# Optimization experiments

Hardware: AMD Instinct MI355X
Metric: run time of the kernel (lower is better)

## Reference

```python
import jax, jax.numpy as jnp
import numpy as np

DIM = 128
WS = 8            # window_size
NH = 4            # num_heads
SHIFT = 4         # shift_size
HD = DIM // NH    # head_dim = 32
SCALE = HD ** (-0.5)
N = WS * WS       # tokens per window = 64


def _rel_pos_index():
    # Static relative-position index, [N, N], values in [0, (2*WS-1)^2)
    coords = np.stack(np.meshgrid(np.arange(WS), np.arange(WS), indexing='ij'))  # [2,WS,WS]
    cf = coords.reshape(2, -1)                                                   # [2,N]
    rel = (cf[:, :, None] - cf[:, None, :]).transpose(1, 2, 0)                   # [N,N,2]
    rel[:, :, 0] += WS - 1
    rel[:, :, 1] += WS - 1
    rel[:, :, 0] *= 2 * WS - 1
    return rel.sum(-1)


def _shift_mask(H, W):
    # Static shifted-window attention mask, [nW, N, N] with 0 / -100 entries
    img = np.zeros((H, W))
    cnt = 0
    for hs in (slice(0, -WS), slice(-WS, -SHIFT), slice(-SHIFT, None)):
        for ws in (slice(0, -WS), slice(-WS, -SHIFT), slice(-SHIFT, None)):
            img[hs, ws] = cnt
            cnt += 1
    mw = img.reshape(H // WS, WS, W // WS, WS).transpose(0, 2, 1, 3).reshape(-1, N)
    am = mw[:, None, :] - mw[:, :, None]
    return np.where(am != 0, -100.0, 0.0).astype(np.float32)


def setup_inputs() -> dict:
    key = jax.random.key(0)
    ks = jax.random.split(key, 5)
    B, H, W = 8, 256, 256
    x = jax.random.normal(ks[0], (B, DIM, H, W), dtype=jnp.float32)
    qkv_w = jax.random.normal(ks[1], (3 * DIM, DIM), dtype=jnp.float32) * (DIM ** -0.5)
    proj_w = jax.random.normal(ks[2], (DIM, DIM), dtype=jnp.float32) * (DIM ** -0.5)
    proj_b = jax.random.normal(ks[3], (DIM,), dtype=jnp.float32) * 0.01
    bias_table = jax.random.normal(ks[4], ((2 * WS - 1) ** 2, NH), dtype=jnp.float32) * 0.02
    return {"x": x, "qkv_w": qkv_w, "proj_w": proj_w, "proj_b": proj_b,
            "bias_table": bias_table}


def reference(x, qkv_w, proj_w, proj_b, bias_table):
    B, C, H, W = x.shape
    # cyclic shift
    x = jnp.roll(x, (-SHIFT, -SHIFT), axis=(2, 3))
    # 1x1 conv qkv == channel matmul
    qkv = jnp.einsum('bchw,oc->bohw', x, qkv_w)  # [B, 3C, H, W]
    nWh, nWw = H // WS, W // WS
    nW = nWh * nWw
    qkv = qkv.reshape(B, 3, NH, HD, nWh, WS, nWw, WS)
    qkv = qkv.transpose(1, 0, 4, 6, 2, 5, 7, 3)          # [3,B,nWh,nWw,NH,WS,WS,HD]
    qkv = qkv.reshape(3, B * nW, NH, N, HD)
    q, k, v = qkv[0], qkv[1], qkv[2]
    attn = jnp.einsum('wnqd,wnkd->wnqk', q, k) * SCALE   # [B*nW, NH, N, N]
    # relative position bias gather
    rpi = _rel_pos_index().reshape(-1)
    bias = bias_table[rpi].reshape(N, N, NH).transpose(2, 0, 1)  # [NH,N,N]
    attn = attn + bias[None]
    # shifted-window mask
    mask = jnp.asarray(_shift_mask(H, W))                # [nW, N, N]
    attn = attn.reshape(B, nW, NH, N, N) + mask[None, :, None]
    attn = jax.nn.softmax(attn, axis=-1).reshape(B * nW, NH, N, N)
    out = jnp.einsum('wnqk,wnkd->wnqd', attn, v)         # [B*nW, NH, N, HD]
    out = out.reshape(B, nWh, nWw, NH, WS, WS, HD)
    out = out.transpose(0, 3, 6, 1, 4, 2, 5).reshape(B, C, H, W)
    out = jnp.einsum('bchw,oc->bohw', out, proj_w) + proj_b[None, :, None, None]
    out = jnp.roll(out, (SHIFT, SHIFT), axis=(2, 3))
    return out
```

## Files before the change

### kernel.cpp

```cpp
#include <hip/hip_runtime.h>

typedef __attribute__((ext_vector_type(8))) short short8;
typedef __attribute__((ext_vector_type(4))) unsigned short ushort4v;
typedef __attribute__((ext_vector_type(4))) float f32x4;

#define SCALE_F 0.17677669529663687f

__device__ __forceinline__ unsigned short f2bf(float f){
  unsigned u = __builtin_bit_cast(unsigned, f);
  u += 0x7fffu + ((u >> 16) & 1u);
  return (unsigned short)(u >> 16);
}
__device__ __forceinline__ float bf2f(unsigned short h){
  unsigned u = ((unsigned)h) << 16;
  return __builtin_bit_cast(float, u);
}


template<bool WSB>
__global__ void __launch_bounds__(256, 2)
swin_fused(const float* __restrict__ x, const float* __restrict__ qkvw_f,
           const float* __restrict__ projw_f, const float* __restrict__ projb,
           const float* __restrict__ btab, const unsigned short* __restrict__ wbf,
           float* __restrict__ out)
{
  __shared__ __align__(16) unsigned char sm[65536];
  const int tid  = threadIdx.x;
  const int lane = tid & 63, wv = tid >> 6;
  const int lr = lane & 15, lg = lane >> 4;

  const int bid = blockIdx.x;
  const int sw  = ((bid & 7) << 10) | (bid >> 3);
  const int b   = sw >> 10;
  const int wh  = (sw >> 5) & 31, ww = sw & 31;
  const int hb  = wh * 8 + 4, wb = ww * 8 + 4;
  const bool h31 = (wh == 31), w31 = (ww == 31);

  {
    const int t  = tid & 63;
    const int gh = (hb + (t >> 3)) & 255;
    const int gw = (wb + (t & 7)) & 255;
    const float* px = x + (((b * 128) << 16) + (gh << 8) + gw);
    const int c0b = (tid >> 6) * 8;
    #pragma unroll
    for (int it = 0; it < 4; ++it) {
      const int c0 = c0b + it * 32;
      const float* p = px + (c0 << 16);
      short8 v;
      #pragma unroll
      for (int cc = 0; cc < 8; ++cc) v[cc] = (short)f2bf(p[cc << 16]);
      *(short8*)(sm + t * 256 + ((2 * c0) ^ ((t & 7) << 4))) = v;
    }
  }
  __syncthreads();

  {
    short8 Bf[16];
    #pragma unroll
    for (int nt = 0; nt < 4; ++nt)
      #pragma unroll
      for (int kk = 0; kk < 4; ++kk) {
        const int t = nt * 16 + lr;
        Bf[nt * 4 + kk] = *(short8*)(sm + t * 256 + ((64 * kk + 16 * lg) ^ ((t & 7) << 4)));
      }
    #pragma unroll
    for (int jj = 0; jj < 6; ++jj) {
      const int mt = wv + 4 * jj;
      const int orow = mt * 16 + lr;
      short8 Af[4];
      #pragma unroll
      for (int kk = 0; kk < 4; ++kk) {
        const int off = orow * 128 + kk * 32 + 8 * lg;
        if constexpr (WSB) {
          Af[kk] = *(const short8*)(wbf + off);
        } else {
          const float* p = qkvw_f + off;
          short8 r;
          #pragma unroll
          for (int e = 0; e < 8; ++e) r[e] = (short)f2bf(p[e]);
          Af[kk] = r;
        }
      }
      f32x4 acc[4];
      #pragma unroll
      for (int nt = 0; nt < 4; ++nt) {
        acc[nt] = (f32x4)(0.f);
        #pragma unroll
        for (int kk = 0; kk < 4; ++kk)
          acc[nt] = __builtin_amdgcn_mfma_f32_16x16x32_bf16(Af[kk], Bf[nt * 4 + kk], acc[nt], 0, 0, 0);
      }
      if (mt < 16) {
        const int base = (mt < 8) ? 16384 : 32768;
        const int c0 = ((mt & 7) * 16) + 4 * lg;
        #pragma unroll
        for (int nt = 0; nt < 4; ++nt) {
          const int t = nt * 16 + lr;
          ushort4v pk;
          #pragma unroll
          for (int r = 0; r < 4; ++r) pk[r] = f2bf(acc[nt][r]);
          *(ushort4v*)(sm + base + t * 256 + ((2 * c0) ^ ((t & 7) << 4))) = pk;
        }
      } else {
        const int c0 = (mt - 16) * 16 + 4 * lg;
        #pragma unroll
        for (int nt = 0; nt < 4; ++nt) {
          const int t = nt * 16 + lr;
          #pragma unroll
          for (int r = 0; r < 4; ++r) {
            const int c = c0 + r;
            *(unsigned short*)(sm + 49152 + c * 128 + ((2 * t) ^ ((c & 7) << 4))) = f2bf(acc[nt][r]);
          }
        }
      }
    }
  }
  __syncthreads();

  f32x4 accpv[8];
  #pragma unroll
  for (int z = 0; z < 8; ++z) accpv[z] = (f32x4)(0.f);

  #pragma unroll
  for (int h = 0; h < 4; ++h) {
    {
      const int cb = 64 * h + 16 * lg;
      const int ktc = wv * 16 + lr;
      const short8 kb = *(short8*)(sm + 32768 + ktc * 256 + (cb ^ ((ktc & 7) << 4)));
      const int ki = ktc >> 3, kj = ktc & 7;
      #pragma unroll
      for (int mt = 0; mt < 4; ++mt) {
        const int q = mt * 16 + lr;
        const short8 qa = *(short8*)(sm + 16384 + q * 256 + (cb ^ ((q & 7) << 4)));
        f32x4 sacc = __builtin_amdgcn_mfma_f32_16x16x32_bf16(qa, kb, (f32x4)(0.f), 0, 0, 0);
        #pragma unroll
        for (int r = 0; r < 4; ++r) {
          const int qrow = mt * 16 + 4 * lg + r;
          const int qi = qrow >> 3, qj = qrow & 7;
          float s = sacc[r] * SCALE_F;
          s += btab[((qi - ki + 7) * 15 + (qj - kj + 7)) * 4 + h];
          const bool bad = (h31 && ((qi >= 4) != (ki >= 4))) || (w31 && ((qj >= 4) != (kj >= 4)));
          s += bad ? -100.f : 0.f;
          *(unsigned short*)(sm + qrow * 128 + ((2 * ktc) ^ ((qrow & 7) << 4))) = f2bf(s);
        }
      }
    }
    __syncthreads();
    {
      const int srow = tid >> 2, sq = tid & 3;
      const int swz = (srow & 7) << 4;
      const short8 s0 = *(short8*)(sm + srow * 128 + ((sq * 32) ^ swz));
      const short8 s1 = *(short8*)(sm + srow * 128 + ((sq * 32 + 16) ^ swz));
      float v[16];
      #pragma unroll
      for (int e = 0; e < 8; ++e) { v[e] = bf2f((unsigned short)s0[e]); v[e + 8] = bf2f((unsigned short)s1[e]); }
      float mx = v[0];
      #pragma unroll
      for (int e = 1; e < 16; ++e) mx = fmaxf(mx, v[e]);
      mx = fmaxf(mx, __shfl_xor(mx, 1));
      mx = fmaxf(mx, __shfl_xor(mx, 2));
      float sum = 0.f;
      #pragma unroll
      for (int e = 0; e < 16; ++e) { v[e] = __expf(v[e] - mx); sum += v[e]; }
      sum += __shfl_xor(sum, 1);
      sum += __shfl_xor(sum, 2);
      const float inv = 1.f / sum;
      short8 p0, p1;
      #pragma unroll
      for (int e = 0; e < 8; ++e) { p0[e] = (short)f2bf(v[e] * inv); p1[e] = (short)f2bf(v[e + 8] * inv); }
      *(short8*)(sm + 8192 + srow * 128 + ((sq * 32) ^ swz)) = p0;
      *(short8*)(sm + 8192 + srow * 128 + ((sq * 32 + 16) ^ swz)) = p1;
    }
    __syncthreads();
    {
      const int q = wv * 16 + lr;
      const int qs_ = (q & 7) << 4;
      const short8 pa0 = *(short8*)(sm + 8192 + q * 128 + ((16 * lg) ^ qs_));
      const short8 pa1 = *(short8*)(sm + 8192 + q * 128 + ((64 + 16 * lg) ^ qs_));
      #pragma unroll
      for (int nd = 0; nd < 2; ++nd) {
        const int c = h * 32 + nd * 16 + lr;
        const int cs = (c & 7) << 4;
        const short8 vb0 = *(short8*)(sm + 49152 + c * 128 + ((16 * lg) ^ cs));
        const short8 vb1 = *(short8*)(sm + 49152 + c * 128 + ((64 + 16 * lg) ^ cs));
        f32x4 a = accpv[h * 2 + nd];
        a = __builtin_amdgcn_mfma_f32_16x16x32_bf16(pa0, vb0, a, 0, 0, 0);
        a = __builtin_amdgcn_mfma_f32_16x16x32_bf16(pa1, vb1, a, 0, 0, 0);
        accpv[h * 2 + nd] = a;
      }
    }
  }

  {
    #pragma unroll
    for (int h = 0; h < 4; ++h)
      #pragma unroll
      for (int nd = 0; nd < 2; ++nd) {
        const int c = h * 32 + nd * 16 + lr;
        const f32x4 a = accpv[h * 2 + nd];
        #pragma unroll
        for (int r = 0; r < 4; ++r) {
          const int t = wv * 16 + 4 * lg + r;
          *(unsigned short*)(sm + 16384 + t * 256 + ((2 * c) ^ ((t & 7) << 4))) = f2bf(a[r]);
        }
      }
  }
  __syncthreads();

  {
    short8 Aa[16];
    #pragma unroll
    for (int mt = 0; mt < 4; ++mt)
      #pragma unroll
      for (int kk = 0; kk < 4; ++kk) {
        const int t = mt * 16 + lr;
        Aa[mt * 4 + kk] = *(short8*)(sm + 16384 + t * 256 + ((64 * kk + 16 * lg) ^ ((t & 7) << 4)));
      }
    #pragma unroll
    for (int ntl = 0; ntl < 2; ++ntl) {
      const int nt = wv + 4 * ntl;
      const int o = nt * 16 + lr;
      short8 Bw[4];
      #pragma unroll
      for (int kk = 0; kk < 4; ++kk) {
        const int coff = kk * 32 + 8 * lg;
        if constexpr (WSB) {
          Bw[kk] = *(const short8*)(wbf + 49152 + o * 128 + coff);
        } else {
          const float* p = projw_f + o * 128 + coff;
          short8 r;
          #pragma unroll
          for (int e = 0; e < 8; ++e) r[e] = (short)f2bf(p[e]);
          Bw[kk] = r;
        }
      }
      const float pb = projb[o];
      #pragma unroll
      for (int mt = 0; mt < 4; ++mt) {
        f32x4 acc = (f32x4)(0.f);
        #pragma unroll
        for (int kk = 0; kk < 4; ++kk)
          acc = __builtin_amdgcn_mfma_f32_16x16x32_bf16(Aa[mt * 4 + kk], Bw[kk], acc, 0, 0, 0);
        const int t0 = mt * 16 + 4 * lg;
        const int gh = (hb + (t0 >> 3)) & 255;
        const int gw0 = (wb + (t0 & 7)) & 255;
        f32x4 ov;
        ov[0] = acc[0] + pb; ov[1] = acc[1] + pb; ov[2] = acc[2] + pb; ov[3] = acc[3] + pb;
        *(f32x4*)(out + (((b * 128 + o) << 16) + (gh << 8) + gw0)) = ov;
      }
    }
  }
}

__global__ void prep_weights(const float* __restrict__ qw, const float* __restrict__ pw,
                             unsigned short* __restrict__ wsb)
{
  const int i = blockIdx.x * 256 + threadIdx.x;
  const int idx = i * 4;
  const float* src = (idx < 49152) ? (qw + idx) : (pw + (idx - 49152));
  f32x4 v = *(const f32x4*)src;
  ushort4v o;
  #pragma unroll
  for (int e = 0; e < 4; ++e) o[e] = f2bf(v[e]);
  *(ushort4v*)(wsb + idx) = o;
}

extern "C" void kernel_launch(void* const* d_in, const int* in_sizes, int n_in,
                              void* d_out, int out_size, void* d_ws, size_t ws_size,
                              hipStream_t stream) {
  const float* x     = (const float*)d_in[0];
  const float* qkvw  = (const float*)d_in[1];
  const float* projw = (const float*)d_in[2];
  const float* projb = (const float*)d_in[3];
  const float* btab  = (const float*)d_in[4];
  float* out = (float*)d_out;

  if (ws_size >= 131072) {
    unsigned short* wsb = (unsigned short*)d_ws;
    prep_weights<<<64, 256, 0, stream>>>(qkvw, projw, wsb);
    swin_fused<true><<<8192, 256, 0, stream>>>(x, qkvw, projw, projb, btab, wsb, out);
  } else {
    swin_fused<false><<<8192, 256, 0, stream>>>(x, qkvw, projw, projb, btab, nullptr, out);
  }
}
```

Measured before the change: 394.3 us.

## Compute QKV per head inside attention loop to shrink LDS and raise occupancy

```diff
diff --git a/kernel.cpp b/kernel.cpp
--- a/kernel.cpp
+++ b/kernel.cpp
@@ -3,8 +3,10 @@
 typedef __attribute__((ext_vector_type(8))) short short8;
 typedef __attribute__((ext_vector_type(4))) unsigned short ushort4v;
 typedef __attribute__((ext_vector_type(4))) float f32x4;
+typedef __attribute__((ext_vector_type(4))) unsigned int uint4v;
 
 #define SCALE_F 0.17677669529663687f
+#define SW(t) ((((t) ^ ((t) >> 3)) & 7) << 4)
 
 __device__ __forceinline__ unsigned short f2bf(float f){
   unsigned u = __builtin_bit_cast(unsigned, f);
@@ -15,16 +17,30 @@
   unsigned u = ((unsigned)h) << 16;
   return __builtin_bit_cast(float, u);
 }
+__device__ __forceinline__ unsigned cvtpk(float a, float b){
+  unsigned w;
+  asm("v_cvt_pk_bf16_f32 %0, %1, %2" : "=v"(w) : "v"(a), "v"(b));
+  return w;
+}
+__device__ __forceinline__ void st_pk4(void* p, f32x4 a){
+  uint2 u; u.x = cvtpk(a[0], a[1]); u.y = cvtpk(a[2], a[3]);
+  *(uint2*)p = u;
+}
 
 
 template<bool WSB>
-__global__ void __launch_bounds__(256, 2)
+__global__ void __launch_bounds__(256, 4)
 swin_fused(const float* __restrict__ x, const float* __restrict__ qkvw_f,
            const float* __restrict__ projw_f, const float* __restrict__ projb,
            const float* __restrict__ btab, const unsigned short* __restrict__ wbf,
            float* __restrict__ out)
 {
-  __shared__ __align__(16) unsigned char sm[65536];
+  __shared__ __align__(16) unsigned char sm[39424];
+  unsigned char* const smq = sm + 16384;
+  unsigned char* const smk = sm + 21504;
+  unsigned char* const smv = sm + 26624;
+  unsigned char* const smS = sm + 31232;
+
   const int tid  = threadIdx.x;
   const int lane = tid & 63, wv = tid >> 6;
   const int lr = lane & 15, lg = lane >> 4;
@@ -37,119 +53,122 @@
   const bool h31 = (wh == 31), w31 = (ww == 31);
 
   {
-    const int t  = tid & 63;
-    const int gh = (hb + (t >> 3)) & 255;
-    const int gw = (wb + (t & 7)) & 255;
-    const float* px = x + (((b * 128) << 16) + (gh << 8) + gw);
-    const int c0b = (tid >> 6) * 8;
-    #pragma unroll
-    for (int it = 0; it < 4; ++it) {
-      const int c0 = c0b + it * 32;
-      const float* p = px + (c0 << 16);
-      short8 v;
-      #pragma unroll
-      for (int cc = 0; cc < 8; ++cc) v[cc] = (short)f2bf(p[cc << 16]);
-      *(short8*)(sm + t * 256 + ((2 * c0) ^ ((t & 7) << 4))) = v;
+    #pragma unroll
+    for (int it = 0; it < 8; ++it) {
+      const int f = tid + 256 * it;
+      const int c    = f >> 4;
+      const int rr   = (f >> 1) & 7;
+      const int half = f & 1;
+      const int gh = (hb + rr) & 255;
+      const int gw = (wb + 4 * half) & 255;
+      const f32x4 v = *(const f32x4*)(x + (((b * 128 + c) << 16) + (gh << 8) + gw));
+      const int t0 = rr * 8 + 4 * half;
+      #pragma unroll
+      for (int e = 0; e < 4; ++e) {
+        const int t = t0 + e;
+        *(unsigned short*)(sm + t * 256 + ((2 * c) ^ SW(t))) = f2bf(v[e]);
+      }
     }
   }
   __syncthreads();
 
-  {
-    short8 Bf[16];
-    #pragma unroll
-    for (int nt = 0; nt < 4; ++nt)
-      #pragma unroll
-      for (int kk = 0; kk < 4; ++kk) {
-        const int t = nt * 16 + lr;
-        Bf[nt * 4 + kk] = *(short8*)(sm + t * 256 + ((64 * kk + 16 * lg) ^ ((t & 7) << 4)));
-      }
-    #pragma unroll
-    for (int jj = 0; jj < 6; ++jj) {
-      const int mt = wv + 4 * jj;
-      const int orow = mt * 16 + lr;
-      short8 Af[4];
-      #pragma unroll
-      for (int kk = 0; kk < 4; ++kk) {
-        const int off = orow * 128 + kk * 32 + 8 * lg;
-        if constexpr (WSB) {
-          Af[kk] = *(const short8*)(wbf + off);
-        } else {
-          const float* p = qkvw_f + off;
-          short8 r;
-          #pragma unroll
-          for (int e = 0; e < 8; ++e) r[e] = (short)f2bf(p[e]);
-          Af[kk] = r;
-        }
-      }
-      f32x4 acc[4];
-      #pragma unroll
-      for (int nt = 0; nt < 4; ++nt) {
-        acc[nt] = (f32x4)(0.f);
-        #pragma unroll
-        for (int kk = 0; kk < 4; ++kk)
-          acc[nt] = __builtin_amdgcn_mfma_f32_16x16x32_bf16(Af[kk], Bf[nt * 4 + kk], acc[nt], 0, 0, 0);
-      }
-      if (mt < 16) {
-        const int base = (mt < 8) ? 16384 : 32768;
-        const int c0 = ((mt & 7) * 16) + 4 * lg;
-        #pragma unroll
-        for (int nt = 0; nt < 4; ++nt) {
-          const int t = nt * 16 + lr;
-          ushort4v pk;
-          #pragma unroll
-          for (int r = 0; r < 4; ++r) pk[r] = f2bf(acc[nt][r]);
-          *(ushort4v*)(sm + base + t * 256 + ((2 * c0) ^ ((t & 7) << 4))) = pk;
-        }
-      } else {
-        const int c0 = (mt - 16) * 16 + 4 * lg;
-        #pragma unroll
-        for (int nt = 0; nt < 4; ++nt) {
-          const int t = nt * 16 + lr;
-          #pragma unroll
-          for (int r = 0; r < 4; ++r) {
-            const int c = c0 + r;
-            *(unsigned short*)(sm + 49152 + c * 128 + ((2 * t) ^ ((c & 7) << 4))) = f2bf(acc[nt][r]);
-          }
-        }
-      }
-    }
-  }
-  __syncthreads();
+  const int ktc = wv * 16 + lr;
+  const int ki = ktc >> 3, kj = ktc & 7;
+  int boff[4][4];
+  #pragma unroll
+  for (int mt = 0; mt < 4; ++mt)
+    #pragma unroll
+    for (int r = 0; r < 4; ++r) {
+      const int qrow = mt * 16 + 4 * lg + r;
+      boff[mt][r] = (((qrow >> 3) - ki + 7) * 15 + ((qrow & 7) - kj + 7)) * 4;
+    }
 
   f32x4 accpv[8];
   #pragma unroll
   for (int z = 0; z < 8; ++z) accpv[z] = (f32x4)(0.f);
 
-  #pragma unroll
+  auto ldx = [&](int t, int kk) -> short8 {
+    return *(const short8*)(sm + t * 256 + ((64 * kk + 16 * lg) ^ SW(t)));
+  };
+  auto ldw8 = [&](const float* wf, const unsigned short* wb16, int row, int kk) -> short8 {
+    const int off = row * 128 + kk * 32 + 8 * lg;
+    if constexpr (WSB) {
+      return *(const short8*)(wb16 + off);
+    } else {
+      const float* p = wf + off;
+      short8 r;
+      #pragma unroll
+      for (int e = 0; e < 8; ++e) r[e] = (short)f2bf(p[e]);
+      return r;
+    }
+  };
+
+  #pragma unroll 1
   for (int h = 0; h < 4; ++h) {
     {
-      const int cb = 64 * h + 16 * lg;
-      const int ktc = wv * 16 + lr;
-      const short8 kb = *(short8*)(sm + 32768 + ktc * 256 + (cb ^ ((ktc & 7) << 4)));
-      const int ki = ktc >> 3, kj = ktc & 7;
+      const int prow0 = ((wv < 2) ? 32 * h : 128 + 32 * h) + 16 * (wv & 1);
+      short8 Af[4];
+      #pragma unroll
+      for (int kk = 0; kk < 4; ++kk) Af[kk] = ldw8(qkvw_f, wbf, prow0 + lr, kk);
+      unsigned char* const dst = (wv < 2) ? smq : smk;
+      #pragma unroll
+      for (int nt = 0; nt < 4; ++nt) {
+        const int t = nt * 16 + lr;
+        f32x4 acc = (f32x4)(0.f);
+        #pragma unroll
+        for (int kk = 0; kk < 4; ++kk)
+          acc = __builtin_amdgcn_mfma_f32_16x16x32_bf16(Af[kk], ldx(t, kk), acc, 0, 0, 0);
+        if (wv < 2) { acc[0] *= SCALE_F; acc[1] *= SCALE_F; acc[2] *= SCALE_F; acc[3] *= SCALE_F; }
+        st_pk4(dst + t * 80 + 32 * (wv & 1) + 8 * lg, acc);
+      }
+      const int vrow0 = 256 + 32 * h + 16 * (wv >> 1);
+      short8 Av[4];
+      #pragma unroll
+      for (int kk = 0; kk < 4; ++kk) Av[kk] = ldw8(qkvw_f, wbf, vrow0 + lr, kk);
+      #pragma unroll
+      for (int ntl = 0; ntl < 2; ++ntl) {
+        const int t = (2 * (wv & 1) + ntl) * 16 + lr;
+        f32x4 acc = (f32x4)(0.f);
+        #pragma unroll
+        for (int kk = 0; kk < 4; ++kk)
+          acc = __builtin_amdgcn_mfma_f32_16x16x32_bf16(Av[kk], ldx(t, kk), acc, 0, 0, 0);
+        const int cb = 16 * (wv >> 1) + 4 * lg;
+        #pragma unroll
+        for (int r = 0; r < 4; ++r)
+          *(unsigned short*)(smv + (cb + r) * 144 + 2 * t) = f2bf(acc[r]);
+      }
+    }
+    __syncthreads();
+
+    {
+      const short8 kb = *(const short8*)(smk + ktc * 80 + 16 * lg);
       #pragma unroll
       for (int mt = 0; mt < 4; ++mt) {
-        const int q = mt * 16 + lr;
-        const short8 qa = *(short8*)(sm + 16384 + q * 256 + (cb ^ ((q & 7) << 4)));
-        f32x4 sacc = __builtin_amdgcn_mfma_f32_16x16x32_bf16(qa, kb, (f32x4)(0.f), 0, 0, 0);
+        const short8 qa = *(const short8*)(smq + (mt * 16 + lr) * 80 + 16 * lg);
+        const f32x4 s = __builtin_amdgcn_mfma_f32_16x16x32_bf16(qa, kb, (f32x4)(0.f), 0, 0, 0);
         #pragma unroll
         for (int r = 0; r < 4; ++r) {
           const int qrow = mt * 16 + 4 * lg + r;
-          const int qi = qrow >> 3, qj = qrow & 7;
-          float s = sacc[r] * SCALE_F;
-          s += btab[((qi - ki + 7) * 15 + (qj - kj + 7)) * 4 + h];
-          const bool bad = (h31 && ((qi >= 4) != (ki >= 4))) || (w31 && ((qj >= 4) != (kj >= 4)));
-          s += bad ? -100.f : 0.f;
-          *(unsigned short*)(sm + qrow * 128 + ((2 * ktc) ^ ((qrow & 7) << 4))) = f2bf(s);
+          float val = s[r] + btab[boff[mt][r] + h];
+          if (h31 | w31) {
+            const int qi = qrow >> 3, qj = qrow & 7;
+            const bool bad = (h31 && ((qi >= 4) != (ki >= 4))) ||
+                             (w31 && ((qj >= 4) != (kj >= 4)));
+            val += bad ? -100.f : 0.f;
+          }
+          *(unsigned short*)(smS + qrow * 128 + ((2 * ktc) ^ SW(qrow))) = f2bf(val);
         }
       }
     }
     __syncthreads();
+
     {
       const int srow = tid >> 2, sq = tid & 3;
-      const int swz = (srow & 7) << 4;
-      const short8 s0 = *(short8*)(sm + srow * 128 + ((sq * 32) ^ swz));
-      const short8 s1 = *(short8*)(sm + srow * 128 + ((sq * 32 + 16) ^ swz));
+      unsigned char* const rp = smS + srow * 128;
+      const int o0 = (32 * sq) ^ SW(srow);
+      const int o1 = (32 * sq + 16) ^ SW(srow);
+      const short8 s0 = *(const short8*)(rp + o0);
+      const short8 s1 = *(const short8*)(rp + o1);
       float v[16];
       #pragma unroll
       for (int e = 0; e < 8; ++e) { v[e] = bf2f((unsigned short)s0[e]); v[e + 8] = bf2f((unsigned short)s1[e]); }
@@ -164,30 +183,32 @@
       sum += __shfl_xor(sum, 1);
       sum += __shfl_xor(sum, 2);
       const float inv = 1.f / sum;
-      short8 p0, p1;
-      #pragma unroll
-      for (int e = 0; e < 8; ++e) { p0[e] = (short)f2bf(v[e] * inv); p1[e] = (short)f2bf(v[e + 8] * inv); }
-      *(short8*)(sm + 8192 + srow * 128 + ((sq * 32) ^ swz)) = p0;
-      *(short8*)(sm + 8192 + srow * 128 + ((sq * 32 + 16) ^ swz)) = p1;
+      uint4v w0, w1;
+      w0.x = cvtpk(v[0] * inv, v[1] * inv);  w0.y = cvtpk(v[2] * inv, v[3] * inv);
+      w0.z = cvtpk(v[4] * inv, v[5] * inv);  w0.w = cvtpk(v[6] * inv, v[7] * inv);
+      w1.x = cvtpk(v[8] * inv, v[9] * inv);  w1.y = cvtpk(v[10] * inv, v[11] * inv);
+      w1.z = cvtpk(v[12] * inv, v[13] * inv); w1.w = cvtpk(v[14] * inv, v[15] * inv);
+      *(uint4v*)(rp + o0) = w0;
+      *(uint4v*)(rp + o1) = w1;
     }
     __syncthreads();
+
     {
       const int q = wv * 16 + lr;
-      const int qs_ = (q & 7) << 4;
-      const short8 pa0 = *(short8*)(sm + 8192 + q * 128 + ((16 * lg) ^ qs_));
-      const short8 pa1 = *(short8*)(sm + 8192 + q * 128 + ((64 + 16 * lg) ^ qs_));
+      const short8 pa0 = *(const short8*)(smS + q * 128 + ((16 * lg) ^ SW(q)));
+      const short8 pa1 = *(const short8*)(smS + q * 128 + ((64 + 16 * lg) ^ SW(q)));
       #pragma unroll
       for (int nd = 0; nd < 2; ++nd) {
-        const int c = h * 32 + nd * 16 + lr;
-        const int cs = (c & 7) << 4;
-        const short8 vb0 = *(short8*)(sm + 49152 + c * 128 + ((16 * lg) ^ cs));
-        const short8 vb1 = *(short8*)(sm + 49152 + c * 128 + ((64 + 16 * lg) ^ cs));
-        f32x4 a = accpv[h * 2 + nd];
+        const int c = nd * 16 + lr;
+        const short8 vb0 = *(const short8*)(smv + c * 144 + 16 * lg);
+        const short8 vb1 = *(const short8*)(smv + c * 144 + 64 + 16 * lg);
+        f32x4 a = accpv[2 * h + nd];
         a = __builtin_amdgcn_mfma_f32_16x16x32_bf16(pa0, vb0, a, 0, 0, 0);
         a = __builtin_amdgcn_mfma_f32_16x16x32_bf16(pa1, vb1, a, 0, 0, 0);
-        accpv[h * 2 + nd] = a;
-      }
-    }
+        accpv[2 * h + nd] = a;
+      }
+    }
+    __syncthreads();
   }
 
   {
@@ -195,12 +216,12 @@
     for (int h = 0; h < 4; ++h)
       #pragma unroll
       for (int nd = 0; nd < 2; ++nd) {
-        const int c = h * 32 + nd * 16 + lr;
-        const f32x4 a = accpv[h * 2 + nd];
+        const int c = 32 * h + nd * 16 + lr;
+        const f32x4 a = accpv[2 * h + nd];
         #pragma unroll
         for (int r = 0; r < 4; ++r) {
           const int t = wv * 16 + 4 * lg + r;
-          *(unsigned short*)(sm + 16384 + t * 256 + ((2 * c) ^ ((t & 7) << 4))) = f2bf(a[r]);
+          *(unsigned short*)(sm + t * 256 + ((2 * c) ^ SW(t))) = f2bf(a[r]);
         }
       }
   }
@@ -213,20 +234,19 @@
       #pragma unroll
       for (int kk = 0; kk < 4; ++kk) {
         const int t = mt * 16 + lr;
-        Aa[mt * 4 + kk] = *(short8*)(sm + 16384 + t * 256 + ((64 * kk + 16 * lg) ^ ((t & 7) << 4)));
+        Aa[mt * 4 + kk] = *(const short8*)(sm + t * 256 + ((64 * kk + 16 * lg) ^ SW(t)));
       }
     #pragma unroll
     for (int ntl = 0; ntl < 2; ++ntl) {
-      const int nt = wv + 4 * ntl;
-      const int o = nt * 16 + lr;
+      const int o = (wv + 4 * ntl) * 16 + lr;
       short8 Bw[4];
       #pragma unroll
       for (int kk = 0; kk < 4; ++kk) {
-        const int coff = kk * 32 + 8 * lg;
+        const int off = o * 128 + kk * 32 + 8 * lg;
         if constexpr (WSB) {
-          Bw[kk] = *(const short8*)(wbf + 49152 + o * 128 + coff);
+          Bw[kk] = *(const short8*)(wbf + 49152 + off);
         } else {
-          const float* p = projw_f + o * 128 + coff;
+          const float* p = projw_f + off;
           short8 r;
           #pragma unroll
           for (int e = 0; e < 8; ++e) r[e] = (short)f2bf(p[e]);
```

Result: slower. 541.4 us (+37.3%).

## Vectorize input loads, change LDS swizzle, hoist proj weights and bias offsets

Applied to the files above, without the earlier changes.

```diff
diff --git a/kernel.cpp b/kernel.cpp
--- a/kernel.cpp
+++ b/kernel.cpp
@@ -5,6 +5,7 @@
 typedef __attribute__((ext_vector_type(4))) float f32x4;
 
 #define SCALE_F 0.17677669529663687f
+#define SW(t) ((((t) ^ ((t) >> 3)) & 7) << 4)
 
 __device__ __forceinline__ unsigned short f2bf(float f){
   unsigned u = __builtin_bit_cast(unsigned, f);
@@ -14,6 +15,15 @@
 __device__ __forceinline__ float bf2f(unsigned short h){
   unsigned u = ((unsigned)h) << 16;
   return __builtin_bit_cast(float, u);
+}
+__device__ __forceinline__ unsigned cvtpk(float a, float b){
+  unsigned w;
+  asm("v_cvt_pk_bf16_f32 %0, %1, %2" : "=v"(w) : "v"(a), "v"(b));
+  return w;
+}
+__device__ __forceinline__ void st_pk4(void* p, f32x4 a){
+  uint2 u; u.x = cvtpk(a[0], a[1]); u.y = cvtpk(a[2], a[3]);
+  *(uint2*)p = u;
 }
 
 
@@ -36,20 +46,43 @@
   const int hb  = wh * 8 + 4, wb = ww * 8 + 4;
   const bool h31 = (wh == 31), w31 = (ww == 31);
 
+  short8 BwH[2][4];
+  float pbH[2];
+  #pragma unroll
+  for (int ntl = 0; ntl < 2; ++ntl) {
+    const int o = (wv + 4 * ntl) * 16 + lr;
+    pbH[ntl] = projb[o];
+    #pragma unroll
+    for (int kk = 0; kk < 4; ++kk) {
+      const int off = o * 128 + kk * 32 + 8 * lg;
+      if constexpr (WSB) {
+        BwH[ntl][kk] = *(const short8*)(wbf + 49152 + off);
+      } else {
+        const float* p = projw_f + off;
+        short8 r;
+        #pragma unroll
+        for (int e = 0; e < 8; ++e) r[e] = (short)f2bf(p[e]);
+        BwH[ntl][kk] = r;
+      }
+    }
+  }
+
   {
-    const int t  = tid & 63;
-    const int gh = (hb + (t >> 3)) & 255;
-    const int gw = (wb + (t & 7)) & 255;
-    const float* px = x + (((b * 128) << 16) + (gh << 8) + gw);
-    const int c0b = (tid >> 6) * 8;
-    #pragma unroll
-    for (int it = 0; it < 4; ++it) {
-      const int c0 = c0b + it * 32;
-      const float* p = px + (c0 << 16);
-      short8 v;
-      #pragma unroll
-      for (int cc = 0; cc < 8; ++cc) v[cc] = (short)f2bf(p[cc << 16]);
-      *(short8*)(sm + t * 256 + ((2 * c0) ^ ((t & 7) << 4))) = v;
+    #pragma unroll
+    for (int it = 0; it < 8; ++it) {
+      const int f = tid + 256 * it;
+      const int c    = f >> 4;
+      const int rr   = (f >> 1) & 7;
+      const int half = f & 1;
+      const int gh = (hb + rr) & 255;
+      const int gw = (wb + 4 * half) & 255;
+      const f32x4 v = *(const f32x4*)(x + (((b * 128 + c) << 16) + (gh << 8) + gw));
+      const int t0 = rr * 8 + 4 * half;
+      #pragma unroll
+      for (int e = 0; e < 4; ++e) {
+        const int t = t0 + e;
+        *(unsigned short*)(sm + t * 256 + ((2 * c) ^ SW(t))) = f2bf(v[e]);
+      }
     }
   }
   __syncthreads();
@@ -61,7 +94,7 @@
       #pragma unroll
       for (int kk = 0; kk < 4; ++kk) {
         const int t = nt * 16 + lr;
-        Bf[nt * 4 + kk] = *(short8*)(sm + t * 256 + ((64 * kk + 16 * lg) ^ ((t & 7) << 4)));
+        Bf[nt * 4 + kk] = *(short8*)(sm + t * 256 + ((64 * kk + 16 * lg) ^ SW(t)));
       }
     #pragma unroll
     for (int jj = 0; jj < 6; ++jj) {
@@ -98,7 +131,7 @@
           ushort4v pk;
           #pragma unroll
           for (int r = 0; r < 4; ++r) pk[r] = f2bf(acc[nt][r]);
-          *(ushort4v*)(sm + base + t * 256 + ((2 * c0) ^ ((t & 7) << 4))) = pk;
+          *(ushort4v*)(sm + base + t * 256 + ((2 * c0) ^ SW(t))) = pk;
         }
       } else {
         const int c0 = (mt - 16) * 16 + 4 * lg;
@@ -108,46 +141,58 @@
           #pragma unroll
           for (int r = 0; r < 4; ++r) {
             const int c = c0 + r;
-            *(unsigned short*)(sm + 49152 + c * 128 + ((2 * t) ^ ((c & 7) << 4))) = f2bf(acc[nt][r]);
+            *(unsigned short*)(sm + 49152 + c * 128 + ((2 * t) ^ SW(c))) = f2bf(acc[nt][r]);
           }
         }
       }
     }
   }
   __syncthreads();
+
+  const int ktc = wv * 16 + lr;
+  const int ki = ktc >> 3, kj = ktc & 7;
+  int boff[4][4];
+  #pragma unroll
+  for (int mt = 0; mt < 4; ++mt)
+    #pragma unroll
+    for (int r = 0; r < 4; ++r) {
+      const int qrow = mt * 16 + 4 * lg + r;
+      boff[mt][r] = (((qrow >> 3) - ki + 7) * 15 + ((qrow & 7) - kj + 7)) * 4;
+    }
 
   f32x4 accpv[8];
   #pragma unroll
   for (int z = 0; z < 8; ++z) accpv[z] = (f32x4)(0.f);
 
-  #pragma unroll
+  #pragma unroll 1
   for (int h = 0; h < 4; ++h) {
     {
       const int cb = 64 * h + 16 * lg;
-      const int ktc = wv * 16 + lr;
-      const short8 kb = *(short8*)(sm + 32768 + ktc * 256 + (cb ^ ((ktc & 7) << 4)));
-      const int ki = ktc >> 3, kj = ktc & 7;
+      const short8 kb = *(short8*)(sm + 32768 + ktc * 256 + (cb ^ SW(ktc)));
       #pragma unroll
       for (int mt = 0; mt < 4; ++mt) {
         const int q = mt * 16 + lr;
-        const short8 qa = *(short8*)(sm + 16384 + q * 256 + (cb ^ ((q & 7) << 4)));
+        const short8 qa = *(short8*)(sm + 16384 + q * 256 + (cb ^ SW(q)));
         f32x4 sacc = __builtin_amdgcn_mfma_f32_16x16x32_bf16(qa, kb, (f32x4)(0.f), 0, 0, 0);
         #pragma unroll
         for (int r = 0; r < 4; ++r) {
           const int qrow = mt * 16 + 4 * lg + r;
-          const int qi = qrow >> 3, qj = qrow & 7;
           float s = sacc[r] * SCALE_F;
-          s += btab[((qi - ki + 7) * 15 + (qj - kj + 7)) * 4 + h];
-          const bool bad = (h31 && ((qi >= 4) != (ki >= 4))) || (w31 && ((qj >= 4) != (kj >= 4)));
-          s += bad ? -100.f : 0.f;
-          *(unsigned short*)(sm + qrow * 128 + ((2 * ktc) ^ ((qrow & 7) << 4))) = f2bf(s);
+          s += btab[boff[mt][r] + h];
+          if (h31 | w31) {
+            const int qi = qrow >> 3, qj = qrow & 7;
+            const bool bad = (h31 && ((qi >= 4) != (ki >= 4))) ||
+                             (w31 && ((qj >= 4) != (kj >= 4)));
+            s += bad ? -100.f : 0.f;
+          }
+          *(unsigned short*)(sm + qrow * 128 + ((2 * ktc) ^ SW(qrow))) = f2bf(s);
         }
       }
     }
     __syncthreads();
     {
       const int srow = tid >> 2, sq = tid & 3;
-      const int swz = (srow & 7) << 4;
+      const int swz = SW(srow);
       const short8 s0 = *(short8*)(sm + srow * 128 + ((sq * 32) ^ swz));
       const short8 s1 = *(short8*)(sm + srow * 128 + ((sq * 32 + 16) ^ swz));
       float v[16];
@@ -173,15 +218,13 @@
     __syncthreads();
     {
       const int q = wv * 16 + lr;
-      const int qs_ = (q & 7) << 4;
-      const short8 pa0 = *(short8*)(sm + 8192 + q * 128 + ((16 * lg) ^ qs_));
-      const short8 pa1 = *(short8*)(sm + 8192 + q * 128 + ((64 + 16 * lg) ^ qs_));
+      const short8 pa0 = *(short8*)(sm + 8192 + q * 128 + ((16 * lg) ^ SW(q)));
+      const short8 pa1 = *(short8*)(sm + 8192 + q * 128 + ((64 + 16 * lg) ^ SW(q)));
       #pragma unroll
       for (int nd = 0; nd < 2; ++nd) {
         const int c = h * 32 + nd * 16 + lr;
-        const int cs = (c & 7) << 4;
-        const short8 vb0 = *(short8*)(sm + 49152 + c * 128 + ((16 * lg) ^ cs));
-        const short8 vb1 = *(short8*)(sm + 49152 + c * 128 + ((64 + 16 * lg) ^ cs));
+        const short8 vb0 = *(short8*)(sm + 49152 + c * 128 + ((16 * lg) ^ SW(c)));
+        const short8 vb1 = *(short8*)(sm + 49152 + c * 128 + ((64 + 16 * lg) ^ SW(c)));
         f32x4 a = accpv[h * 2 + nd];
         a = __builtin_amdgcn_mfma_f32_16x16x32_bf16(pa0, vb0, a, 0, 0, 0);
         a = __builtin_amdgcn_mfma_f32_16x16x32_bf16(pa1, vb1, a, 0, 0, 0);
@@ -200,7 +243,7 @@
         #pragma unroll
         for (int r = 0; r < 4; ++r) {
           const int t = wv * 16 + 4 * lg + r;
-          *(unsigned short*)(sm + 16384 + t * 256 + ((2 * c) ^ ((t & 7) << 4))) = f2bf(a[r]);
+          *(unsigned short*)(sm + 16384 + t * 256 + ((2 * c) ^ SW(t))) = f2bf(a[r]);
         }
       }
   }
@@ -213,33 +256,18 @@
       #pragma unroll
       for (int kk = 0; kk < 4; ++kk) {
         const int t = mt * 16 + lr;
-        Aa[mt * 4 + kk] = *(short8*)(sm + 16384 + t * 256 + ((64 * kk + 16 * lg) ^ ((t & 7) << 4)));
+        Aa[mt * 4 + kk] = *(short8*)(sm + 16384 + t * 256 + ((64 * kk + 16 * lg) ^ SW(t)));
       }
     #pragma unroll
     for (int ntl = 0; ntl < 2; ++ntl) {
-      const int nt = wv + 4 * ntl;
-      const int o = nt * 16 + lr;
-      short8 Bw[4];
-      #pragma unroll
-      for (int kk = 0; kk < 4; ++kk) {
-        const int coff = kk * 32 + 8 * lg;
-        if constexpr (WSB) {
-          Bw[kk] = *(const short8*)(wbf + 49152 + o * 128 + coff);
-        } else {
-          const float* p = projw_f + o * 128 + coff;
-          short8 r;
-          #pragma unroll
-          for (int e = 0; e < 8; ++e) r[e] = (short)f2bf(p[e]);
-          Bw[kk] = r;
-        }
-      }
-      const float pb = projb[o];
+      const int o = (wv + 4 * ntl) * 16 + lr;
+      const float pb = pbH[ntl];
       #pragma unroll
       for (int mt = 0; mt < 4; ++mt) {
         f32x4 acc = (f32x4)(0.f);
         #pragma unroll
         for (int kk = 0; kk < 4; ++kk)
-          acc = __builtin_amdgcn_mfma_f32_16x16x32_bf16(Aa[mt * 4 + kk], Bw[kk], acc, 0, 0, 0);
+          acc = __builtin_amdgcn_mfma_f32_16x16x32_bf16(Aa[mt * 4 + kk], BwH[ntl][kk], acc, 0, 0, 0);
         const int t0 = mt * 16 + 4 * lg;
         const int gh = (hb + (t0 >> 3)) & 255;
         const int gw0 = (wb + (t0 & 7)) & 255;
```

Result: slower. 415.8 us (+5.4%).
